# Optimization experiments

Hardware: AMD Instinct MI355X
Metric: run time of the kernel (lower is better)

## Reference

```python
import jax, jax.numpy as jnp
import numpy as np
from jax import lax

FI, FO, K, EPS = 512, 256, 3, 1e-06


def _fir_kernel(gain):
    f = jnp.array([1.0, 3.0, 3.0, 1.0], dtype=jnp.float32)
    f = f[None, :] * f[:, None]
    f = f / f.sum() * gain  # (4,4), symmetric so conv-vs-correlation flip is a no-op
    return f


def setup_inputs() -> dict:
    key = jax.random.key(0)
    k1, k2 = jax.random.split(key)
    x = jax.random.normal(k1, (8, FI, 64, 64), dtype=jnp.float32)
    w = jax.random.normal(k2, (1, FO, FI, K, K), dtype=jnp.float32)
    return {"x": x, "w": w}


def reference(x, w):
    w_scale = (FI * K * K) ** (-0.5)
    wm = w[0] * w_scale  # (fo, fi, k, k); per-sample scale is constant across batch
    demod = lax.rsqrt(jnp.sum(wm * wm, axis=(1, 2, 3)) + EPS)  # (fo,)
    wm = wm * demod[:, None, None, None]
    # torch conv_transpose2d(stride=2, padding=0) with weight (fi, fo, k, k) where
    # weight[i, o] = wm[o, i]  ==  dilated conv with kernel flip(wm) OIHW, pad k-1=2.
    kern = wm[:, :, ::-1, ::-1]
    y = lax.conv_general_dilated(
        x, kern, window_strides=(1, 1), padding=[(2, 2), (2, 2)],
        lhs_dilation=(2, 2), dimension_numbers=("NCHW", "OIHW", "NCHW"))
    # upFirDn2D with scale=2, conv_k=3: p=0 -> pad (1,1) both dims, filter gain 4
    f = _fir_kernel(4.0)
    C = y.shape[1]
    fk = jnp.broadcast_to(f[None, None], (C, 1, 4, 4))
    y = lax.conv_general_dilated(
        y, fk, window_strides=(1, 1), padding=[(1, 1), (1, 1)],
        feature_group_count=C, dimension_numbers=("NCHW", "OIHW", "NCHW"))
    return y  # (8, 256, 128, 128)
```

## Files before the change

### kernel.cpp

```cpp
#include <hip/hip_runtime.h>

typedef unsigned short u16;
typedef unsigned int u32;
typedef __attribute__((ext_vector_type(8))) short bf16x8;
typedef __attribute__((ext_vector_type(4))) float f32x4;

#define XP_BYTES 35684352
#define YB_BYTES 68714544
#define HY_OFF   (XP_BYTES + YB_BYTES)
#define WS_NEED  ((size_t)HY_OFF + 2359296)
#define CS 16776

__device__ inline u16 f2bf(float f) {
  union { float f; unsigned u; } v; v.f = f;
  unsigned r = v.u + 0x7fffu + ((v.u >> 16) & 1u);
  return (u16)(r >> 16);
}

__device__ inline void gl_lds16(const u16* g, u16* l) {
  __builtin_amdgcn_global_load_lds(
      (const __attribute__((address_space(1))) unsigned int*)g,
      (__attribute__((address_space(3))) unsigned int*)l, 16, 0, 0);
}

__global__ void xprep(const float* __restrict__ x, u16* __restrict__ xp) {
  __shared__ float tile[64 * 65];
  int bid = blockIdx.x;
  int cc = bid & 7, h = (bid >> 3) & 63, n = bid >> 9;
  int c0 = cc * 64;
  int t = threadIdx.x;
  const float* xb = x + ((size_t)(n * 512 + c0) * 64 + h) * 64;
  for (int r = 0; r < 16; ++r) {
    int flat = r * 256 + t;
    int ci = flat >> 6, w = flat & 63;
    tile[w * 65 + ci] = xb[(size_t)ci * 4096 + w];
  }
  __syncthreads();
  u16* xpb = xp + ((size_t)(n * 66 + h + 1) * 66 + 1) * 512 + c0;
  for (int r = 0; r < 8; ++r) {
    int flat = r * 256 + t;
    int pr = flat & 31;
    int w = flat >> 5;
    int ci = pr * 2;
    float v0 = tile[w * 65 + ci], v1 = tile[w * 65 + ci + 1];
    unsigned pk = (unsigned)f2bf(v0) | ((unsigned)f2bf(v1) << 16);
    *(unsigned*)(xpb + (size_t)w * 512 + ci) = pk;
  }
  u16* rowbase = xp + ((size_t)(n * 66 + h + 1) * 66) * 512 + c0;
  if (t < 32) *(u32*)(rowbase + 2 * t) = 0u;
  else if (t < 64) *(u32*)(rowbase + (size_t)65 * 512 + 2 * (t - 32)) = 0u;
  if (h == 0) {
    u16* r0 = xp + ((size_t)(n * 66) * 66) * 512 + c0;
    for (int j = t; j < 2112; j += 256) {
      int col = j >> 5, wi = j & 31;
      *(u32*)(r0 + (size_t)col * 512 + 2 * wi) = 0u;
    }
  }
  if (h == 63) {
    u16* r65 = xp + ((size_t)(n * 66 + 65) * 66) * 512 + c0;
    for (int j = t; j < 2112; j += 256) {
      int col = j >> 5, wi = j & 31;
      *(u32*)(r65 + (size_t)col * 512 + 2 * wi) = 0u;
    }
  }
}

__global__ void wprep9(const float* __restrict__ w, u16* __restrict__ Hy) {
  __shared__ float wl[4608];
  __shared__ float red[256];
  int o = blockIdx.x, t = threadIdx.x;
  const float* wo = w + (size_t)o * 4608;
  float s = 0.f;
  for (int j = t; j < 4608; j += 256) { float v = wo[j]; wl[j] = v; s += v * v; }
  red[t] = s;
  __syncthreads();
  for (int st = 128; st; st >>= 1) { if (t < st) red[t] += red[t + st]; __syncthreads(); }
  float demod = rsqrtf(red[0] * (1.0f / 4608.0f) + 1e-6f);
  float scale = demod * 0.014731391274719739f;
  const int DY[9] = {0, 2, 0, 2, 0, 2, 1, 1, 1};
  const int DX[9] = {0, 0, 2, 2, 1, 1, 0, 2, 1};
  for (int i = t; i < 512; i += 256) {
#pragma unroll
    for (int pl = 0; pl < 9; ++pl) {
      float g = wl[i * 9 + DY[pl] * 3 + DX[pl]] * scale;
      Hy[(size_t)pl * 131072 + (size_t)o * 512 + i] = f2bf(g);
    }
  }
}

__global__ __launch_bounds__(256) void conv_y(const u16* __restrict__ xp,
                                              const u16* __restrict__ Hy,
                                              u16* __restrict__ yb) {
  __shared__ __align__(16) u16 su[17408];

  int bid = blockIdx.x;
  int t = threadIdx.x;
  int wave = t >> 6, lane = t & 63;

  int mt, nt, img, Wp, CNT, NTAP, PB, PO, STLIM, rp, rq;
  if (bid < 544)       { int L = bid;        mt = L % 34; int r2 = L / 34; nt = r2 & 1; img = r2 >> 1; Wp = 66; CNT = 4290; NTAP = 4; PB = 0; PO = 0;     STLIM = 4296; rp = 0; rq = 0; }
  else if (bid < 1072) { int L = bid - 544;  mt = L % 33; int r2 = L / 33; nt = r2 & 1; img = r2 >> 1; Wp = 64; CNT = 4160; NTAP = 2; PB = 4; PO = 4296;  STLIM = 4160; rp = 0; rq = 1; }
  else if (bid < 1600) { int L = bid - 1072; mt = L % 33; int r2 = L / 33; nt = r2 & 1; img = r2 >> 1; Wp = 66; CNT = 4224; NTAP = 2; PB = 6; PO = 8456;  STLIM = 4224; rp = 1; rq = 0; }
  else                 { int L = bid - 1600; mt = L % 32; int r2 = L / 32; nt = r2 & 1; img = r2 >> 1; Wp = 64; CNT = 4096; NTAP = 1; PB = 8; PO = 12680; STLIM = 4096; rp = 1; rq = 1; }

  int m0 = mt * 128;
  int o0 = nt * 128;
  int wm0 = (wave & 1) * 64;
  int wn0 = (wave >> 1) * 64;
  int la = lane & 15, grp = lane >> 4;

  int rho = t >> 3;
  int gch = (t & 7) ^ (rho & 7);

  u32 gA[4];
#pragma unroll
  for (int i = 0; i < 4; ++i) {
    int m = m0 + rho + i * 32;
    if (m > CNT - 1) m = CNT - 1;
    int a = m / (u32)Wp;
    int b = m - a * Wp;
    gA[i] = (u32)(((img * 66 + a + 1) * 66 + (b + 1)) * 512 + gch * 8);
  }
  u32 gB[4];
#pragma unroll
  for (int i = 0; i < 4; ++i)
    gB[i] = (u32)((o0 + i * 32 + rho) * 512 + gch * 8);

  f32x4 acc[4][4];
#pragma unroll
  for (int i = 0; i < 4; ++i)
#pragma unroll
    for (int j = 0; j < 4; ++j) acc[i][j] = (f32x4){0.f, 0.f, 0.f, 0.f};

  for (int tap = 0; tap < NTAP; ++tap) {
    int du, dv;
    if (rp == 0 && rq == 0)      { du = tap & 1; dv = tap >> 1; }
    else if (rp == 0)            { du = tap;     dv = 0; }
    else if (rq == 0)            { du = 0;       dv = tap; }
    else                         { du = 0;       dv = 0; }
    u32 tapadj = (u32)((du * 66 + dv) * 512);
    const u16* hp = Hy + (size_t)(PB + tap) * 131072;

#pragma unroll 1
    for (int kc = 0; kc < 8; ++kc) {
      u32 ko = (u32)(kc * 64);
      __syncthreads();
#pragma unroll
      for (int i = 0; i < 4; ++i)
        gl_lds16(xp + (gA[i] - tapadj + ko), su + i * 2048 + wave * 512);
#pragma unroll
      for (int i = 0; i < 4; ++i)
        gl_lds16(hp + (gB[i] + ko), su + 8192 + i * 2048 + wave * 512);
      __syncthreads();

#pragma unroll
      for (int ksub = 0; ksub < 2; ++ksub) {
        bf16x8 af[4], bf[4];
#pragma unroll
        for (int ti = 0; ti < 4; ++ti) {
          int row = wm0 + ti * 16 + la;
          int ch = (ksub * 4 + grp) ^ (row & 7);
          af[ti] = *(const bf16x8*)(su + row * 64 + ch * 8);
        }
#pragma unroll
        for (int tj = 0; tj < 4; ++tj) {
          int row = wn0 + tj * 16 + la;
          int ch = (ksub * 4 + grp) ^ (row & 7);
          bf[tj] = *(const bf16x8*)(su + 8192 + row * 64 + ch * 8);
        }
#pragma unroll
        for (int ti = 0; ti < 4; ++ti)
#pragma unroll
          for (int tj = 0; tj < 4; ++tj)
            acc[ti][tj] = __builtin_amdgcn_mfma_f32_16x16x32_bf16(
                af[ti], bf[tj], acc[ti][tj], 0, 0, 0);
      }
    }
  }

  __syncthreads();
#pragma unroll
  for (int tj = 0; tj < 4; ++tj) {
    int orow = wn0 + tj * 16 + la;
#pragma unroll
    for (int ti = 0; ti < 4; ++ti)
#pragma unroll
      for (int jp = 0; jp < 2; ++jp) {
        int ml = wm0 + ti * 16 + grp * 4 + jp * 2;
        u32 pk = (u32)f2bf(acc[ti][tj][jp * 2]) |
                 ((u32)f2bf(acc[ti][tj][jp * 2 + 1]) << 16);
        *(u32*)(su + orow * 136 + ml) = pk;
      }
  }
  __syncthreads();
  {
    u16* ybp = yb + 8;
    int o = t >> 1, s = t & 1;
    size_t gb = (size_t)(img * 256 + o0 + o) * CS + PO + m0 + s * 64;
#pragma unroll
    for (int i = 0; i < 8; ++i) {
      int mo = s * 64 + i * 8;
      if (m0 + mo < STLIM)
        *(bf16x8*)(ybp + gb + i * 8) = *(const bf16x8*)(su + o * 136 + mo);
    }
  }
}

__global__ void fir2(const u16* __restrict__ yb, float* __restrict__ z) {
  int flat = blockIdx.x * 256 + threadIdx.x;
  int qh = flat & 15, phb = (flat >> 4) & 31, o = (flat >> 9) & 255, n = flat >> 17;
  const u16* cb = yb + 8 + (size_t)(n * 256 + o) * CS;
  int a0 = 2 * phb - 1;
  int b0 = 4 * qh - 1;

  float out[4][8];
#pragma unroll
  for (int i = 0; i < 4; ++i)
#pragma unroll
    for (int j = 0; j < 8; ++j) out[i][j] = 0.f;

  const int PO_[4] = {0, 4296, 8456, 12680};
  const int WP_[4] = {66, 64, 66, 64};
  const int HA_[4] = {65, 65, 64, 64};
  const int WB_[4] = {65, 64, 65, 64};

#pragma unroll
  for (int ph = 0; ph < 4; ++ph) {
    int rp = ph >> 1, rq = ph & 1;
    const u16* pb = cb + PO_[ph];
    float hcol[4][8];
#pragma unroll
    for (int la = 0; la < 4; ++la) {
      if (rp == 0 && la == 0) continue;
      int ag = a0 + la;
      bool rv = (ag >= 0) && (ag < HA_[ph]);
      const u16* rb = pb + (ag * WP_[ph] + b0 - 1);
      u32 ls[4];
      ls[0] = *(const u32*)(rb);
      ls[1] = *(const u32*)(rb + 2);
      ls[2] = *(const u32*)(rb + 4);
      ls[3] = *(const u32*)(rb + 6);
      float v[6];
#pragma unroll
      for (int lb = 0; lb < 6; ++lb) {
        int jj = lb + 1;
        u32 w16 = (jj & 1) ? (ls[jj >> 1] >> 16) : (ls[jj >> 1] & 0xffffu);
        float fv = __uint_as_float(w16 << 16);
        int bg = b0 + lb;
        bool ok = rv && (bg >= 0) && (bg < WB_[ph]);
        v[lb] = ok ? fv : 0.f;
      }
#pragma unroll
      for (int e = 0; e < 4; ++e) {
        if (rq == 0) {
          hcol[la][2 * e]     = 3.f * v[e + 1] + v[e + 2];
          hcol[la][2 * e + 1] = v[e + 1] + 3.f * v[e + 2];
        } else {
          hcol[la][2 * e]     = v[e] + 3.f * v[e + 1];
          hcol[la][2 * e + 1] = 3.f * v[e + 1] + v[e + 2];
        }
      }
    }
#pragma unroll
    for (int jq = 0; jq < 8; ++jq) {
      if (rp == 0) {
        out[0][jq] += 3.f * hcol[1][jq] + hcol[2][jq];
        out[1][jq] += hcol[1][jq] + 3.f * hcol[2][jq];
        out[2][jq] += 3.f * hcol[2][jq] + hcol[3][jq];
        out[3][jq] += hcol[2][jq] + 3.f * hcol[3][jq];
      } else {
        out[0][jq] += hcol[0][jq] + 3.f * hcol[1][jq];
        out[1][jq] += 3.f * hcol[1][jq] + hcol[2][jq];
        out[2][jq] += hcol[1][jq] + 3.f * hcol[2][jq];
        out[3][jq] += 3.f * hcol[2][jq] + hcol[3][jq];
      }
    }
  }

  float* zb = z + ((size_t)(n * 256 + o) * 128 + phb * 4) * 128 + qh * 8;
#pragma unroll
  for (int ip = 0; ip < 4; ++ip) {
    f32x4 v0, v1;
#pragma unroll
    for (int j = 0; j < 4; ++j) { v0[j] = out[ip][j] * 0.0625f; v1[j] = out[ip][j + 4] * 0.0625f; }
    *(f32x4*)(zb + (size_t)ip * 128) = v0;
    *(f32x4*)(zb + (size_t)ip * 128 + 4) = v1;
  }
}

__global__ void wprep36(const float* __restrict__ w, u16* __restrict__ Hm) {
  __shared__ float wl[4608];
  __shared__ float red[256];
  int o = blockIdx.x, t = threadIdx.x;
  const float* wo = w + (size_t)o * 4608;
  float s = 0.f;
  for (int j = t; j < 4608; j += 256) { float v = wo[j]; wl[j] = v; s += v * v; }
  red[t] = s;
  __syncthreads();
  for (int st = 128; st; st >>= 1) { if (t < st) red[t] += red[t + st]; __syncthreads(); }
  float demod = rsqrtf(red[0] * (1.0f / 4608.0f) + 1e-6f);
  float scale = demod * 0.014731391274719739f;
  const float F1[4] = {1.f, 3.f, 3.f, 1.f};
  for (int i = t; i < 512; i += 256) {
    float wm[9];
    for (int k = 0; k < 9; ++k) wm[k] = wl[i * 9 + k] * scale;
    for (int rp = 0; rp < 2; ++rp)
      for (int rq = 0; rq < 2; ++rq)
        for (int u = 0; u < 3; ++u)
          for (int v = 0; v < 3; ++v) {
            int s_ = 2 - 2 * u + rp, t_ = 2 - 2 * v + rq;
            float g = 0.f;
            for (int dy = 0; dy < 3; ++dy) {
              int a = dy + 1 - s_;
              if (a < 0 || a > 3) continue;
              for (int dx = 0; dx < 3; ++dx) {
                int b = dx + 1 - t_;
                if (b < 0 || b > 3) continue;
                g += wm[dy * 3 + dx] * (F1[a] * F1[b]);
              }
            }
            g *= 0.0625f;
            Hm[(size_t)((rp * 2 + rq) * 9 + u * 3 + v) * 131072 + (size_t)o * 512 + i] = f2bf(g);
          }
  }
}

__global__ __launch_bounds__(256) void conv_main(const u16* __restrict__ xp,
                                                 const u16* __restrict__ Hm,
                                                 float* __restrict__ z) {
  __shared__ __align__(16) float smemf[8448];
  u16* su = (u16*)smemf;
  int bid = blockIdx.x;
  int sub = bid & 7;
  int rp = sub >> 2;
  int o0 = (sub & 3) * 64;
  int mtile = bid >> 3;
  int n_img = mtile >> 5;
  int hp0 = (mtile & 31) * 2;
  int t = threadIdx.x;
  int wave = t >> 6, lane = t & 63;
  int wm0 = (wave & 1) * 64;
  int wn0 = (wave >> 1) * 32;
  int la = lane & 15;
  int ks = (lane >> 4) * 8;
  int rsel = t >> 2;
  int koff = (t & 3) * 8;
  f32x4 acc[2][4][2];
#pragma unroll
  for (int a = 0; a < 2; ++a)
#pragma unroll
    for (int b = 0; b < 4; ++b)
#pragma unroll
      for (int c = 0; c < 2; ++c)
        acc[a][b][c] = (f32x4){0.f, 0.f, 0.f, 0.f};
#pragma unroll 1
  for (int tap = 0; tap < 9; ++tap) {
    int du = tap / 3, dv = tap - du * 3;
    const u16* gA0 = xp + ((size_t)(n_img * 66 + hp0 + du) * 66 + dv) * 512;
    const u16* gB0 = Hm + (size_t)(rp * 18 + tap) * 131072 + (size_t)(o0 + rsel) * 512 + koff;
    const u16* gAr0 = gA0 + (size_t)rsel * 512 + koff;
    const u16* gAr1 = gA0 + (size_t)(66 + rsel) * 512 + koff;
#pragma unroll 1
    for (int kc = 0; kc < 16; ++kc) {
      int c0 = kc * 32;
      __syncthreads();
      gl_lds16(gAr0 + c0, su + wave * 512);
      gl_lds16(gAr1 + c0, su + 2048 + wave * 512);
      gl_lds16(gB0 + c0,              su + 4096 + wave * 512);
      gl_lds16(gB0 + 9 * 131072 + c0, su + 6144 + wave * 512);
      __syncthreads();
      bf16x8 af[4];
#pragma unroll
      for (int ti = 0; ti < 4; ++ti)
        af[ti] = *(const bf16x8*)(su + (wm0 + ti * 16 + la) * 32 + ks);
      bf16x8 bfr[2][2];
#pragma unroll
      for (int rqq = 0; rqq < 2; ++rqq)
#pragma unroll
        for (int tj = 0; tj < 2; ++tj)
          bfr[rqq][tj] = *(const bf16x8*)(su + 4096 + rqq * 2048 + (wn0 + tj * 16 + la) * 32 + ks);
#pragma unroll
      for (int rqq = 0; rqq < 2; ++rqq)
#pragma unroll
        for (int ti = 0; ti < 4; ++ti)
#pragma unroll
          for (int tj = 0; tj < 2; ++tj)
            acc[rqq][ti][tj] = __builtin_amdgcn_mfma_f32_16x16x32_bf16(
                af[ti], bfr[rqq][tj], acc[rqq][ti][tj], 0, 0, 0);
    }
  }
  __syncthreads();
  float* lws = smemf + wave * 2112;
  int p = 2 * (hp0 + (wave & 1)) + rp;
#pragma unroll
  for (int tj = 0; tj < 2; ++tj) {
#pragma unroll
    for (int rqq = 0; rqq < 2; ++rqq)
#pragma unroll
      for (int ti = 0; ti < 4; ++ti) {
        int wqb = ti * 16 + (lane >> 4) * 4;
        f32x4 v = acc[rqq][ti][tj];
#pragma unroll
        for (int r = 0; r < 4; ++r)
          lws[la * 132 + 2 * (wqb + r) + rqq] = v[r];
      }
    __syncthreads();
    int obase = o0 + wn0 + tj * 16;
#pragma unroll
    for (int c = 0; c < 8; ++c) {
      int idx = c * 64 + lane;
      int ol = idx >> 5, q4 = (idx & 31) * 4;
      f32x4 vv = *(const f32x4*)(lws + ol * 132 + q4);
      *(f32x4*)(z + (((size_t)n_img * 256 + obase + ol) * 128 + p) * 128 + q4) = vv;
    }
    __syncthreads();
  }
}

extern "C" void kernel_launch(void* const* d_in, const int* in_sizes, int n_in,
                              void* d_out, int out_size, void* d_ws, size_t ws_size,
                              hipStream_t stream) {
  const float* x = (const float*)d_in[0];
  const float* w = (const float*)d_in[1];
  float* z = (float*)d_out;
  u16* xp = (u16*)d_ws;

  if (ws_size >= WS_NEED) {
    u16* yb = (u16*)((char*)d_ws + XP_BYTES);
    u16* hy = (u16*)((char*)d_ws + HY_OFF);
    xprep<<<4096, 256, 0, stream>>>(x, xp);
    wprep9<<<256, 256, 0, stream>>>(w, hy);
    conv_y<<<2112, 256, 0, stream>>>(xp, hy, yb);
    fir2<<<4096, 256, 0, stream>>>(yb, z);
  } else {
    u16* Hm = (u16*)((char*)d_ws + XP_BYTES);
    hipMemsetAsync(xp, 0, XP_BYTES, stream);
    xprep<<<4096, 256, 0, stream>>>(x, xp);
    wprep36<<<256, 256, 0, stream>>>(w, Hm);
    conv_main<<<2048, 256, 0, stream>>>(xp, Hm, z);
  }
}
```

Before: 332.1 us.

## Rewrite conv_y as 256x256-tile, 8-wave, double-buffered pipelined MFMA GEMM

Restructures the polyphase transposed-conv GEMM so each 512-thread block computes a 256x256 output tile (all output channels) instead of 128x128. Global-to-LDS loads run into a double-buffered 128KB shared region and are interleaved with quarter-tile MFMA groups using explicit waitcnt, barriers and setprio. The goal is to hide load latency and halve redundant A/B reloads. The epilogue uses an XOR-swizzled LDS staging layout. This trades occupancy and a smaller grid (536 blocks) for more reuse and overlap, and the hand-written sync is fragile.

```diff
diff --git a/kernel.cpp b/kernel.cpp
--- a/kernel.cpp
+++ b/kernel.cpp
@@ -88,120 +88,210 @@
   }
 }
 
-__global__ __launch_bounds__(256) void conv_y(const u16* __restrict__ xp,
-                                              const u16* __restrict__ Hy,
-                                              u16* __restrict__ yb) {
-  __shared__ __align__(16) u16 su[17408];
+#define BARR() __builtin_amdgcn_s_barrier()
+#define WAITL() do { asm volatile("s_waitcnt lgkmcnt(0)" ::: "memory"); __builtin_amdgcn_sched_barrier(0); } while (0)
+#define WAITV4() do { asm volatile("s_waitcnt vmcnt(4)" ::: "memory"); __builtin_amdgcn_sched_barrier(0); } while (0)
+#define WAITV0() do { asm volatile("s_waitcnt vmcnt(0)" ::: "memory"); __builtin_amdgcn_sched_barrier(0); } while (0)
+
+__device__ __forceinline__ void rdA8(const u16* sb, int rbase, int grp, bf16x8 af[4][2]) {
+#pragma unroll
+  for (int ti = 0; ti < 4; ++ti) {
+    int r = rbase + ti * 16;
+    int x7 = r & 7;
+#pragma unroll
+    for (int ks = 0; ks < 2; ++ks) {
+      int ch = (ks * 4 + grp) ^ x7;
+      af[ti][ks] = *(const bf16x8*)(sb + r * 64 + ch * 8);
+    }
+  }
+}
+
+__device__ __forceinline__ void rdB4(const u16* sb, int rbase, int grp, bf16x8 bfr[2][2]) {
+#pragma unroll
+  for (int tj = 0; tj < 2; ++tj) {
+    int r = rbase + tj * 16;
+    int x7 = r & 7;
+#pragma unroll
+    for (int ks = 0; ks < 2; ++ks) {
+      int ch = (ks * 4 + grp) ^ x7;
+      bfr[tj][ks] = *(const bf16x8*)(sb + 16384 + r * 64 + ch * 8);
+    }
+  }
+}
+
+template <int MI, int NI>
+__device__ __forceinline__ void qmfma(const bf16x8 af[4][2], const bf16x8 bfr[2][2],
+                                      f32x4 acc[8][4]) {
+#pragma unroll
+  for (int ti = 0; ti < 4; ++ti)
+#pragma unroll
+    for (int tj = 0; tj < 2; ++tj)
+#pragma unroll
+      for (int ks = 0; ks < 2; ++ks)
+        acc[MI * 4 + ti][NI * 2 + tj] = __builtin_amdgcn_mfma_f32_16x16x32_bf16(
+            af[ti][ks], bfr[tj][ks], acc[MI * 4 + ti][NI * 2 + tj], 0, 0, 0);
+}
+
+__device__ __forceinline__ void stA2(const u16* __restrict__ xp, u16* d0, u16* d1,
+                                     int tile, int NK, u32 a0, u32 a1,
+                                     u32 adj1, u32 adj2, u32 adj3) {
+  if (tile < NK) {
+    int tap = tile >> 3;
+    u32 ko = (u32)((tile & 7) << 6);
+    u32 adj = tap == 0 ? 0u : (tap == 1 ? adj1 : (tap == 2 ? adj2 : adj3));
+    gl_lds16(xp + (a0 - adj + ko), d0);
+    gl_lds16(xp + (a1 - adj + ko), d1);
+  }
+}
+
+__device__ __forceinline__ void stB2(const u16* __restrict__ hb, u16* d0, u16* d1,
+                                     int tile, int NK, u32 b0, u32 b1) {
+  if (tile < NK) {
+    int tap = tile >> 3;
+    u32 ko = (u32)((tile & 7) << 6);
+    const u16* hp = hb + (size_t)tap * 131072;
+    gl_lds16(hp + (b0 + ko), d0);
+    gl_lds16(hp + (b1 + ko), d1);
+  }
+}
+
+__global__ __launch_bounds__(512, 2) void conv_y(const u16* __restrict__ xp,
+                                                 const u16* __restrict__ Hy,
+                                                 u16* __restrict__ yb) {
+  __shared__ __align__(16) u16 su[65536];
 
   int bid = blockIdx.x;
   int t = threadIdx.x;
-  int wave = t >> 6, lane = t & 63;
-
-  int mt, nt, img, Wp, CNT, NTAP, PB, PO, STLIM, rp, rq;
-  if (bid < 544)       { int L = bid;        mt = L % 34; int r2 = L / 34; nt = r2 & 1; img = r2 >> 1; Wp = 66; CNT = 4290; NTAP = 4; PB = 0; PO = 0;     STLIM = 4296; rp = 0; rq = 0; }
-  else if (bid < 1072) { int L = bid - 544;  mt = L % 33; int r2 = L / 33; nt = r2 & 1; img = r2 >> 1; Wp = 64; CNT = 4160; NTAP = 2; PB = 4; PO = 4296;  STLIM = 4160; rp = 0; rq = 1; }
-  else if (bid < 1600) { int L = bid - 1072; mt = L % 33; int r2 = L / 33; nt = r2 & 1; img = r2 >> 1; Wp = 66; CNT = 4224; NTAP = 2; PB = 6; PO = 8456;  STLIM = 4224; rp = 1; rq = 0; }
-  else                 { int L = bid - 1600; mt = L % 32; int r2 = L / 32; nt = r2 & 1; img = r2 >> 1; Wp = 64; CNT = 4096; NTAP = 1; PB = 8; PO = 12680; STLIM = 4096; rp = 1; rq = 1; }
-
-  int m0 = mt * 128;
-  int o0 = nt * 128;
-  int wm0 = (wave & 1) * 64;
-  int wn0 = (wave >> 1) * 64;
+  int wid = t >> 6, lane = t & 63;
+
+  int img = bid & 7;
+  int kk = bid >> 3;
+  int mt, Wp, CNT, NTAP, PB, PO, STLIM;
+  u32 adj1 = 0, adj2 = 0, adj3 = 0;
+  if (kk < 17)      { mt = kk;      Wp = 66; CNT = 4290; NTAP = 4; PB = 0; PO = 0;     STLIM = 4296;
+                      adj1 = 33792u; adj2 = 512u; adj3 = 34304u; }
+  else if (kk < 34) { mt = kk - 17; Wp = 64; CNT = 4160; NTAP = 2; PB = 4; PO = 4296;  STLIM = 4160;
+                      adj1 = 33792u; }
+  else if (kk < 51) { mt = kk - 34; Wp = 66; CNT = 4224; NTAP = 2; PB = 6; PO = 8456;  STLIM = 4224;
+                      adj1 = 512u; }
+  else              { mt = kk - 51; Wp = 64; CNT = 4096; NTAP = 1; PB = 8; PO = 12680; STLIM = 4096; }
+
+  int m0 = mt * 256;
+  int NK = NTAP * 8;
+  int NITER = NTAP * 4;
+  const u16* hb = Hy + (size_t)PB * 131072;
+
+  int wm = wid >> 2, wn = wid & 3;
   int la = lane & 15, grp = lane >> 4;
 
   int rho = t >> 3;
   int gch = (t & 7) ^ (rho & 7);
 
-  u32 gA[4];
+  u32 gA[4], gB[4];
 #pragma unroll
   for (int i = 0; i < 4; ++i) {
-    int m = m0 + rho + i * 32;
+    int m = m0 + i * 64 + rho;
     if (m > CNT - 1) m = CNT - 1;
-    int a = m / (u32)Wp;
-    int b = m - a * Wp;
+    u32 a = (u32)m / (u32)Wp;
+    u32 b = (u32)m - a * (u32)Wp;
     gA[i] = (u32)(((img * 66 + a + 1) * 66 + (b + 1)) * 512 + gch * 8);
-  }
-  u32 gB[4];
-#pragma unroll
-  for (int i = 0; i < 4; ++i)
-    gB[i] = (u32)((o0 + i * 32 + rho) * 512 + gch * 8);
-
-  f32x4 acc[4][4];
-#pragma unroll
-  for (int i = 0; i < 4; ++i)
+    gB[i] = (u32)((i * 64 + rho) * 512 + gch * 8);
+  }
+  u16* sw = su + wid * 512;
+
+  f32x4 acc[8][4];
+#pragma unroll
+  for (int i = 0; i < 8; ++i)
 #pragma unroll
     for (int j = 0; j < 4; ++j) acc[i][j] = (f32x4){0.f, 0.f, 0.f, 0.f};
 
-  for (int tap = 0; tap < NTAP; ++tap) {
-    int du, dv;
-    if (rp == 0 && rq == 0)      { du = tap & 1; dv = tap >> 1; }
-    else if (rp == 0)            { du = tap;     dv = 0; }
-    else if (rq == 0)            { du = 0;       dv = tap; }
-    else                         { du = 0;       dv = 0; }
-    u32 tapadj = (u32)((du * 66 + dv) * 512);
-    const u16* hp = Hy + (size_t)(PB + tap) * 131072;
+  stB2(hb, sw + 16384, sw + 20480, 0, NK, gB[0], gB[1]);
+  stB2(hb, sw + 24576, sw + 28672, 0, NK, gB[2], gB[3]);
+  stA2(xp, sw, sw + 4096, 0, NK, gA[0], gA[1], adj1, adj2, adj3);
+  stA2(xp, sw + 8192, sw + 12288, 0, NK, gA[2], gA[3], adj1, adj2, adj3);
+  stB2(hb, sw + 49152, sw + 53248, 1, NK, gB[0], gB[1]);
+  stB2(hb, sw + 57344, sw + 61440, 1, NK, gB[2], gB[3]);
+  WAITV4();
+  BARR();
+
+  bf16x8 af[4][2], bf0[2][2], bf1[2][2];
 
 #pragma unroll 1
-    for (int kc = 0; kc < 8; ++kc) {
-      u32 ko = (u32)(kc * 64);
-      __syncthreads();
-#pragma unroll
-      for (int i = 0; i < 4; ++i)
-        gl_lds16(xp + (gA[i] - tapadj + ko), su + i * 2048 + wave * 512);
-#pragma unroll
-      for (int i = 0; i < 4; ++i)
-        gl_lds16(hp + (gB[i] + ko), su + 8192 + i * 2048 + wave * 512);
-      __syncthreads();
-
-#pragma unroll
-      for (int ksub = 0; ksub < 2; ++ksub) {
-        bf16x8 af[4], bf[4];
-#pragma unroll
-        for (int ti = 0; ti < 4; ++ti) {
-          int row = wm0 + ti * 16 + la;
-          int ch = (ksub * 4 + grp) ^ (row & 7);
-          af[ti] = *(const bf16x8*)(su + row * 64 + ch * 8);
-        }
-#pragma unroll
-        for (int tj = 0; tj < 4; ++tj) {
-          int row = wn0 + tj * 16 + la;
-          int ch = (ksub * 4 + grp) ^ (row & 7);
-          bf[tj] = *(const bf16x8*)(su + 8192 + row * 64 + ch * 8);
-        }
-#pragma unroll
-        for (int ti = 0; ti < 4; ++ti)
-#pragma unroll
-          for (int tj = 0; tj < 4; ++tj)
-            acc[ti][tj] = __builtin_amdgcn_mfma_f32_16x16x32_bf16(
-                af[ti], bf[tj], acc[ti][tj], 0, 0, 0);
-      }
-    }
-  }
-
+  for (int it = 0; it < NITER; ++it) {
+    int t0 = 2 * it;
+    bool more = (it + 1 < NITER);
+
+    rdA8(su, wm * 128 + la, grp, af);
+    rdB4(su, wn * 64 + la, grp, bf0);
+    stA2(xp, sw + 32768, sw + 36864, t0 + 1, NK, gA[0], gA[1], adj1, adj2, adj3);
+    BARR(); WAITL();
+    __builtin_amdgcn_s_setprio(1); qmfma<0, 0>(af, bf0, acc); __builtin_amdgcn_s_setprio(0);
+    BARR();
+    rdB4(su, wn * 64 + 32 + la, grp, bf1);
+    stA2(xp, sw + 40960, sw + 45056, t0 + 1, NK, gA[2], gA[3], adj1, adj2, adj3);
+    BARR(); WAITL();
+    __builtin_amdgcn_s_setprio(1); qmfma<0, 1>(af, bf1, acc); __builtin_amdgcn_s_setprio(0);
+    BARR();
+    rdA8(su, wm * 128 + 64 + la, grp, af);
+    stB2(hb, sw + 16384, sw + 20480, t0 + 2, NK, gB[0], gB[1]);
+    BARR(); WAITL();
+    __builtin_amdgcn_s_setprio(1); qmfma<1, 1>(af, bf1, acc); __builtin_amdgcn_s_setprio(0);
+    BARR();
+    stB2(hb, sw + 24576, sw + 28672, t0 + 2, NK, gB[2], gB[3]);
+    BARR(); WAITL();
+    __builtin_amdgcn_s_setprio(1); qmfma<1, 0>(af, bf0, acc); __builtin_amdgcn_s_setprio(0);
+    if (more) { WAITV4(); } else { WAITV0(); }
+    BARR();
+    rdA8(su + 32768, wm * 128 + la, grp, af);
+    rdB4(su + 32768, wn * 64 + la, grp, bf0);
+    stA2(xp, sw, sw + 4096, t0 + 2, NK, gA[0], gA[1], adj1, adj2, adj3);
+    BARR(); WAITL();
+    __builtin_amdgcn_s_setprio(1); qmfma<0, 0>(af, bf0, acc); __builtin_amdgcn_s_setprio(0);
+    BARR();
+    rdB4(su + 32768, wn * 64 + 32 + la, grp, bf1);
+    stA2(xp, sw + 8192, sw + 12288, t0 + 2, NK, gA[2], gA[3], adj1, adj2, adj3);
+    BARR(); WAITL();
+    __builtin_amdgcn_s_setprio(1); qmfma<0, 1>(af, bf1, acc); __builtin_amdgcn_s_setprio(0);
+    BARR();
+    rdA8(su + 32768, wm * 128 + 64 + la, grp, af);
+    stB2(hb, sw + 49152, sw + 53248, t0 + 3, NK, gB[0], gB[1]);
+    BARR(); WAITL();
+    __builtin_amdgcn_s_setprio(1); qmfma<1, 1>(af, bf1, acc); __builtin_amdgcn_s_setprio(0);
+    BARR();
+    stB2(hb, sw + 57344, sw + 61440, t0 + 3, NK, gB[2], gB[3]);
+    BARR(); WAITL();
+    __builtin_amdgcn_s_setprio(1); qmfma<1, 0>(af, bf0, acc); __builtin_amdgcn_s_setprio(0);
+    if (more) { WAITV4(); }
+    BARR();
+  }
+
+  WAITV0();
   __syncthreads();
 #pragma unroll
-  for (int tj = 0; tj < 4; ++tj) {
-    int orow = wn0 + tj * 16 + la;
-#pragma unroll
-    for (int ti = 0; ti < 4; ++ti)
+  for (int nj = 0; nj < 4; ++nj) {
+    int orow = wn * 64 + nj * 16 + la;
+    int x7 = orow & 7;
+#pragma unroll
+    for (int mi8 = 0; mi8 < 8; ++mi8)
 #pragma unroll
       for (int jp = 0; jp < 2; ++jp) {
-        int ml = wm0 + ti * 16 + grp * 4 + jp * 2;
-        u32 pk = (u32)f2bf(acc[ti][tj][jp * 2]) |
-                 ((u32)f2bf(acc[ti][tj][jp * 2 + 1]) << 16);
-        *(u32*)(su + orow * 136 + ml) = pk;
+        int ml = wm * 128 + mi8 * 16 + grp * 4 + jp * 2;
+        u32 pk = (u32)f2bf(acc[mi8][nj][jp * 2]) |
+                 ((u32)f2bf(acc[mi8][nj][jp * 2 + 1]) << 16);
+        *(u32*)(su + orow * 256 + (((ml >> 3) ^ x7) * 8) + (ml & 7)) = pk;
       }
   }
   __syncthreads();
   {
     u16* ybp = yb + 8;
     int o = t >> 1, s = t & 1;
-    size_t gb = (size_t)(img * 256 + o0 + o) * CS + PO + m0 + s * 64;
-#pragma unroll
-    for (int i = 0; i < 8; ++i) {
-      int mo = s * 64 + i * 8;
+    size_t gb = (size_t)(img * 256 + o) * CS + PO + m0 + s * 128;
+    int x7 = o & 7;
+#pragma unroll
+    for (int i = 0; i < 16; ++i) {
+      int mo = s * 128 + i * 8;
       if (m0 + mo < STLIM)
-        *(bf16x8*)(ybp + gb + i * 8) = *(const bf16x8*)(su + o * 136 + mo);
+        *(bf16x8*)(ybp + gb + i * 8) = *(const bf16x8*)(su + o * 256 + (((mo >> 3) ^ x7) * 8));
     }
   }
 }
@@ -430,7 +520,7 @@
     u16* hy = (u16*)((char*)d_ws + HY_OFF);
     xprep<<<4096, 256, 0, stream>>>(x, xp);
     wprep9<<<256, 256, 0, stream>>>(w, hy);
-    conv_y<<<2112, 256, 0, stream>>>(xp, hy, yb);
+    conv_y<<<536, 512, 0, stream>>>(xp, hy, yb);
     fir2<<<4096, 256, 0, stream>>>(yb, z);
   } else {
     u16* Hm = (u16*)((char*)d_ws + XP_BYTES);
```

New measurement: 315.0 us. -5.1%, faster.
